# Optimization experiments

Measured on AMD Instinct MI355X. Metric: run time of the kernel, lower is better.

## Reference

```python
import jax, jax.numpy as jnp
import numpy as np
import math

B, S, D = 4, 4096, 2048
HEAD_DIM = 128  # dim_model // head_nums = 2048 // 16
DEPTH = 12


def setup_inputs() -> dict:
    key = jax.random.key(0)
    ks = jax.random.split(key, 8)
    std = 0.1
    return {
        "x": jax.random.normal(ks[0], (B, S, D), dtype=jnp.float32),
        "WQ": jax.random.normal(ks[1], (D, 2 * HEAD_DIM), dtype=jnp.float32) * (D ** -0.5),
        "WK": jax.random.normal(ks[2], (D, 2 * HEAD_DIM), dtype=jnp.float32) * (D ** -0.5),
        "WV": jax.random.normal(ks[3], (D, 2 * HEAD_DIM), dtype=jnp.float32) * (D ** -0.5),
        "lambda_q1": jax.random.normal(ks[4], (HEAD_DIM,), dtype=jnp.float32) * std,
        "lambda_q2": jax.random.normal(ks[5], (HEAD_DIM,), dtype=jnp.float32) * std,
        "lambda_k1": jax.random.normal(ks[6], (HEAD_DIM,), dtype=jnp.float32) * std,
        "lambda_k2": jax.random.normal(ks[7], (HEAD_DIM,), dtype=jnp.float32) * std,
    }


def reference(x, WQ, WK, WV, lambda_q1, lambda_q2, lambda_k1, lambda_k2):
    scale = HEAD_DIM ** -0.5
    lambda_init = 0.8 - 0.6 * math.exp(-0.3 * DEPTH)

    q = x @ WQ                      # [B, S, 2*hd]
    k = x @ WK
    v = x @ WV                      # [B, S, 2*hd]
    q1, q2 = q[..., :HEAD_DIM], q[..., HEAD_DIM:]
    k1, k2 = k[..., :HEAD_DIM], k[..., HEAD_DIM:]

    a1 = jnp.einsum("bqd,bkd->bqk", q1, k1) * scale  # [B, S, S]
    a2 = jnp.einsum("bqd,bkd->bqk", q2, k2) * scale

    lambda_1 = jnp.exp(jnp.sum(lambda_q1 * lambda_k1))
    lambda_2 = jnp.exp(jnp.sum(lambda_q2 * lambda_k2))
    lam = lambda_1 + lambda_2 + lambda_init

    attn = jax.nn.softmax(a1, axis=-1) - lam * jax.nn.softmax(a2, axis=-1)
    return jnp.einsum("bqk,bkd->bqd", attn, v)  # [B, S, 2*hd]
```

## Files before the change

### kernel.cpp

```cpp
#include <hip/hip_runtime.h>
#include <stdint.h>

typedef unsigned short u16;
typedef __attribute__((ext_vector_type(4))) float f32x4;
typedef __attribute__((ext_vector_type(16))) float f32x16;
typedef __attribute__((ext_vector_type(8))) short s16x8;
typedef __attribute__((ext_vector_type(8))) __bf16 bf16x8;
typedef __attribute__((ext_vector_type(8))) unsigned short u16x8;
typedef __attribute__((ext_vector_type(4))) unsigned short u16x4;
typedef __attribute__((ext_vector_type(4))) uint32_t u32x4;

__device__ __forceinline__ f32x4 mfma16(s16x8 a, s16x8 b, f32x4 c) {
  return __builtin_amdgcn_mfma_f32_16x16x32_bf16(
      __builtin_bit_cast(bf16x8, a), __builtin_bit_cast(bf16x8, b), c, 0, 0, 0);
}
__device__ __forceinline__ f32x16 mfma32(s16x8 a, s16x8 b, f32x16 c) {
  return __builtin_amdgcn_mfma_f32_32x32x16_bf16(
      __builtin_bit_cast(bf16x8, a), __builtin_bit_cast(bf16x8, b), c, 0, 0, 0);
}

__device__ __forceinline__ void gl_lds16(const u16* g, u16* l) {
  __builtin_amdgcn_global_load_lds(
      (const __attribute__((address_space(1))) void*)g,
      (__attribute__((address_space(3))) void*)l, 16, 0, 0);
}

__device__ __forceinline__ u16 bf16rne(float f) {
  uint32_t u = __builtin_bit_cast(uint32_t, f);
  u += 0x7fffu + ((u >> 16) & 1u);
  return (u16)(u >> 16);
}

__global__ void cast_x_kernel(const float* __restrict__ x, u16* __restrict__ xb) {
  size_t i = ((size_t)blockIdx.x * 256 + threadIdx.x) * 8;
  f32x4 a = *(const f32x4*)(x + i);
  f32x4 b = *(const f32x4*)(x + i + 4);
  u16x8 o;
#pragma unroll
  for (int j = 0; j < 4; ++j) { o[j] = bf16rne(a[j]); o[4 + j] = bf16rne(b[j]); }
  *(u16x8*)(xb + i) = o;
}

__global__ void cast_w_kernel(const float* __restrict__ WQ, const float* __restrict__ WK,
                              const float* __restrict__ WV, u16* __restrict__ Wt, float qscale) {
  int i = blockIdx.x * 256 + threadIdx.x;
  int r = i >> 11, k = i & 2047;
  int sel = r >> 8, c = r & 255;
  const float* W = (sel == 0) ? WQ : (sel == 1) ? WK : WV;
  float v = W[(size_t)k * 256 + c];
  if (sel == 0) v *= qscale;
  Wt[i] = bf16rne(v);
}

__global__ __launch_bounds__(256) void proj_gemm(const u16* __restrict__ xb, const u16* __restrict__ Wt,
                                                 u16* __restrict__ Qb, u16* __restrict__ Kb,
                                                 u16* __restrict__ Vt) {
  const int bid = blockIdx.x;
  const int xcd = bid & 7, j = bid >> 3;
  const int m0 = (xcd * 16 + (j / 6)) * 128;
  const int n0 = (j % 6) * 128;
  const int tid = threadIdx.x, lane = tid & 63, w = tid >> 6;
  const int ln = lane & 15, quad = lane >> 4;
  const int wm = w & 1, wn = w >> 1;
  __shared__ __align__(16) u16 As[128 * 32];
  __shared__ __align__(16) u16 Bs[128 * 32];
  f32x4 acc[4][4];
#pragma unroll
  for (int i = 0; i < 4; ++i)
#pragma unroll
    for (int jj = 0; jj < 4; ++jj) acc[i][jj] = f32x4{0.f, 0.f, 0.f, 0.f};

  for (int kk = 0; kk < 2048; kk += 32) {
    __syncthreads();
#pragma unroll
    for (int i = 0; i < 2; ++i) {
      int p = tid + i * 256;
      int row = p >> 2, cg = (p & 3) ^ (row & 3);
      gl_lds16(xb + (size_t)(m0 + row) * 2048 + kk + cg * 8, As + (size_t)(p - lane) * 8);
      gl_lds16(Wt + (size_t)(n0 + row) * 2048 + kk + cg * 8, Bs + (size_t)(p - lane) * 8);
    }
    __syncthreads();
    s16x8 a[4];
#pragma unroll
    for (int mt = 0; mt < 4; ++mt) {
      int r = wm * 64 + mt * 16 + ln;
      a[mt] = *(const s16x8*)(As + r * 32 + ((quad ^ (r & 3)) * 8));
    }
#pragma unroll
    for (int nt = 0; nt < 4; ++nt) {
      int r = wn * 64 + nt * 16 + ln;
      s16x8 bf = *(const s16x8*)(Bs + r * 32 + ((quad ^ (r & 3)) * 8));
#pragma unroll
      for (int mt = 0; mt < 4; ++mt) acc[mt][nt] = mfma16(a[mt], bf, acc[mt][nt]);
    }
  }
#pragma unroll
  for (int mt = 0; mt < 4; ++mt)
#pragma unroll
    for (int nt = 0; nt < 4; ++nt) {
      int row0 = m0 + wm * 64 + mt * 16 + quad * 4;
      int col = n0 + wn * 64 + nt * 16 + ln;
      int sel = col >> 8, c = col & 255;
      u16x4 vv;
#pragma unroll
      for (int jj = 0; jj < 4; ++jj) vv[jj] = bf16rne(acc[mt][nt][jj]);
      if (sel == 2) {
        int b = row0 >> 12, s = row0 & 4095;
        *(u16x4*)(Vt + (size_t)b * 1048576 + (size_t)c * 4096 + s) = vv;
      } else {
        u16* dst = (sel == 0) ? Qb : Kb;
#pragma unroll
        for (int jj = 0; jj < 4; ++jj) dst[(size_t)(row0 + jj) * 256 + c] = vv[jj];
      }
    }
}

__global__ void lam_kernel(const float* __restrict__ lq1, const float* __restrict__ lq2,
                           const float* __restrict__ lk1, const float* __restrict__ lk2,
                           float* __restrict__ lamp) {
  int t = threadIdx.x;
  float d1 = lq1[t] * lk1[t] + lq1[t + 64] * lk1[t + 64];
  float d2 = lq2[t] * lk2[t] + lq2[t + 64] * lk2[t + 64];
#pragma unroll
  for (int off = 32; off; off >>= 1) {
    d1 += __shfl_xor(d1, off);
    d2 += __shfl_xor(d2, off);
  }
  if (t == 0) *lamp = expf(d1) + expf(d2) + (0.8f - 0.6f * expf(-3.6f));
}

__global__ __launch_bounds__(256, 2) void attn_kernel(const u16* __restrict__ Qb,
                                                      const u16* __restrict__ Kb,
                                                      const u16* __restrict__ Vt,
                                                      const float* __restrict__ lamp,
                                                      float* __restrict__ out) {
  const int bid = blockIdx.x;
  const int xcd = bid & 7;
  const int b = xcd >> 1;
  const int qt = ((bid >> 3) << 1) + (xcd & 1);
  const int tid = threadIdx.x, lane = tid & 63, w = tid >> 6;
  const int l5 = lane & 31, lh = lane >> 5;
  const int m = w & 1, kt = w >> 1;

  __shared__ __align__(16) char smem[68096];
  u16* Ks = (u16*)smem;
  u16* Vs = (u16*)(smem + 32768);
  float* buf0 = (float*)smem;
  float* buf1 = (float*)(smem + 33792);
  float* ls = (float*)(smem + 67584);

  s16x8 bq[8];
  {
    const u16* qp = Qb + ((size_t)(b * 4096 + qt * 32 + l5)) * 256 + m * 128 + lh * 8;
#pragma unroll
    for (int s = 0; s < 8; ++s) bq[s] = *(const s16x8*)(qp + s * 16);
  }

  f32x16 O[8];
#pragma unroll
  for (int ct = 0; ct < 8; ++ct)
#pragma unroll
    for (int r = 0; r < 16; ++r) O[ct][r] = 0.f;
  float l_run = 0.f;

  const u16* Kg0 = Kb + ((size_t)b * 4096) * 256;
  const u16* Vg0 = Vt + (size_t)b * 1048576;

  for (int kb = 0; kb < 4096; kb += 64) {
    __syncthreads();
#pragma unroll
    for (int i = 0; i < 8; ++i) {
      int p = tid + i * 256;
      int row = p >> 5, c = p & 31;
      int cg = (c & 16) | ((c ^ row) & 15);
      gl_lds16(Kg0 + (size_t)(kb + row) * 256 + cg * 8, Ks + (size_t)(p - lane) * 8);
    }
#pragma unroll
    for (int i = 0; i < 8; ++i) {
      int p = tid + i * 256;
      int row = p >> 3, c = p & 7;
      int cg = c ^ (row & 7);
      gl_lds16(Vg0 + (size_t)row * 4096 + kb + cg * 8, Vs + (size_t)(p - lane) * 8);
    }
    __syncthreads();

    f32x16 Sa, Sb;
#pragma unroll
    for (int r = 0; r < 16; ++r) { Sa[r] = 0.f; Sb[r] = 0.f; }
#pragma unroll
    for (int s = 0; s < 8; s += 2) {
      int row = kt * 32 + l5;
      int c0 = m * 16 + s * 2 + lh;
      int c1 = m * 16 + (s + 1) * 2 + lh;
      s16x8 a0 = *(const s16x8*)(Ks + row * 256 + (((c0 & 16) | ((c0 ^ row) & 15))) * 8);
      s16x8 a1 = *(const s16x8*)(Ks + row * 256 + (((c1 & 16) | ((c1 ^ row) & 15))) * 8);
      Sa = mfma32(a0, bq[s], Sa);
      Sb = mfma32(a1, bq[s + 1], Sb);
    }

    uint32_t P[8];
#pragma unroll
    for (int d = 0; d < 8; ++d) {
      float p0 = exp2f(Sa[2 * d] + Sb[2 * d]);
      float p1 = exp2f(Sa[2 * d + 1] + Sb[2 * d + 1]);
      l_run += p0 + p1;
      P[d] = (uint32_t)bf16rne(p0) | ((uint32_t)bf16rne(p1) << 16);
    }
    uint32_t X[8];
#pragma unroll
    for (int d = 0; d < 8; ++d) X[d] = (uint32_t)__shfl_xor((int)P[d], 32);

#pragma unroll
    for (int ks = 0; ks < 2; ++ks) {
      u32x4 fd;
      fd[0] = lh ? X[ks * 4 + 2] : P[ks * 4 + 0];
      fd[1] = lh ? X[ks * 4 + 3] : P[ks * 4 + 1];
      fd[2] = lh ? P[ks * 4 + 2] : X[ks * 4 + 0];
      fd[3] = lh ? P[ks * 4 + 3] : X[ks * 4 + 1];
      s16x8 pf = __builtin_bit_cast(s16x8, fd);
      int c = (kt * 32 + ks * 16) / 8 + lh;
#pragma unroll
      for (int ct = 0; ct < 8; ++ct) {
        int row = ct * 32 + l5;
        s16x8 vf = *(const s16x8*)(Vs + row * 64 + ((c ^ (row & 7)) * 8));
        O[ct] = mfma32(vf, pf, O[ct]);
      }
    }
  }

  float lam = *lamp;
  l_run += __shfl_xor(l_run, 32);
  __syncthreads();
  if (lane < 32) ls[(m * 2 + kt) * 32 + l5] = l_run;
  float* bufm = m ? buf1 : buf0;
  if (kt == 1) {
#pragma unroll
    for (int ct = 0; ct < 8; ++ct)
#pragma unroll
      for (int r = 0; r < 16; ++r) {
        int vcol = ct * 32 + (r & 3) + 8 * (r >> 2) + 4 * lh;
        bufm[vcol * 33 + l5] = O[ct][r];
      }
  }
  __syncthreads();
  if (kt == 0) {
    float linv = 1.f / (ls[(m * 2) * 32 + l5] + ls[(m * 2 + 1) * 32 + l5]);
#pragma unroll
    for (int ct = 0; ct < 8; ++ct)
#pragma unroll
      for (int r = 0; r < 16; ++r) {
        int vcol = ct * 32 + (r & 3) + 8 * (r >> 2) + 4 * lh;
        bufm[vcol * 33 + l5] = (O[ct][r] + bufm[vcol * 33 + l5]) * linv;
      }
  }
  __syncthreads();
  float* og = out + ((size_t)(b * 4096 + qt * 32)) * 256;
#pragma unroll
  for (int j2 = 0; j2 < 32; ++j2) {
    float v = buf0[tid * 33 + j2] - lam * buf1[tid * 33 + j2];
    og[(size_t)j2 * 256 + tid] = v;
  }
}

extern "C" void kernel_launch(void* const* d_in, const int* in_sizes, int n_in,
                              void* d_out, int out_size, void* d_ws, size_t ws_size,
                              hipStream_t stream) {
  (void)in_sizes; (void)n_in; (void)out_size; (void)ws_size;
  const float* x   = (const float*)d_in[0];
  const float* WQ  = (const float*)d_in[1];
  const float* WK  = (const float*)d_in[2];
  const float* WV  = (const float*)d_in[3];
  const float* lq1 = (const float*)d_in[4];
  const float* lq2 = (const float*)d_in[5];
  const float* lk1 = (const float*)d_in[6];
  const float* lk2 = (const float*)d_in[7];
  float* out = (float*)d_out;

  char* ws = (char*)d_ws;
  u16* xb = (u16*)ws;   ws += (size_t)16384 * 2048 * 2;
  u16* Wt = (u16*)ws;   ws += (size_t)768 * 2048 * 2;
  u16* Qb = (u16*)ws;   ws += (size_t)16384 * 256 * 2;
  u16* Kb = (u16*)ws;   ws += (size_t)16384 * 256 * 2;
  u16* Vt = (u16*)ws;   ws += (size_t)16384 * 256 * 2;
  float* lamp = (float*)ws;

  const float qscale = 0.0883883476f * 1.44269504f;

  hipLaunchKernelGGL(cast_x_kernel, dim3(16384), dim3(256), 0, stream, x, xb);
  hipLaunchKernelGGL(cast_w_kernel, dim3(6144), dim3(256), 0, stream, WQ, WK, WV, Wt, qscale);
  hipLaunchKernelGGL(proj_gemm, dim3(768), dim3(256), 0, stream, xb, Wt, Qb, Kb, Vt);
  hipLaunchKernelGGL(lam_kernel, dim3(1), dim3(64), 0, stream, lq1, lq2, lk1, lk2, lamp);
  hipLaunchKernelGGL(attn_kernel, dim3(512), dim3(256), 0, stream, Qb, Kb, Vt, lamp, out);
}
```

Measured before the change: 442.6 us.

## Double-buffer K/V tiles in LDS, prefetch V fragments, use permlane32_swap

Splits LDS into two 64KB stages so the next K/V tile is fetched with global_load_lds while the current one is computed, leaving one barrier per iteration. V fragments are loaded from LDS into registers before the softmax exp so LDS latency overlaps the exp work. The P transpose across the lane halves uses permlane32_swap instead of shfl_xor plus selects. Launch bounds drop to one block per CU because of the larger LDS footprint and the extra registers, which lowers occupancy.

```diff
diff --git a/kernel.cpp b/kernel.cpp
--- a/kernel.cpp
+++ b/kernel.cpp
@@ -9,6 +9,7 @@
 typedef __attribute__((ext_vector_type(8))) unsigned short u16x8;
 typedef __attribute__((ext_vector_type(4))) unsigned short u16x4;
 typedef __attribute__((ext_vector_type(4))) uint32_t u32x4;
+typedef __attribute__((ext_vector_type(2))) uint32_t u32x2;
 
 __device__ __forceinline__ f32x4 mfma16(s16x8 a, s16x8 b, f32x4 c) {
   return __builtin_amdgcn_mfma_f32_16x16x32_bf16(
@@ -129,7 +130,7 @@
   if (t == 0) *lamp = expf(d1) + expf(d2) + (0.8f - 0.6f * expf(-3.6f));
 }
 
-__global__ __launch_bounds__(256, 2) void attn_kernel(const u16* __restrict__ Qb,
+__global__ __launch_bounds__(256, 1) void attn_kernel(const u16* __restrict__ Qb,
                                                       const u16* __restrict__ Kb,
                                                       const u16* __restrict__ Vt,
                                                       const float* __restrict__ lamp,
@@ -142,32 +143,17 @@
   const int l5 = lane & 31, lh = lane >> 5;
   const int m = w & 1, kt = w >> 1;
 
-  __shared__ __align__(16) char smem[68096];
-  u16* Ks = (u16*)smem;
-  u16* Vs = (u16*)(smem + 32768);
+  __shared__ __align__(16) char smem[131072];
   float* buf0 = (float*)smem;
   float* buf1 = (float*)(smem + 33792);
   float* ls = (float*)(smem + 67584);
 
-  s16x8 bq[8];
-  {
-    const u16* qp = Qb + ((size_t)(b * 4096 + qt * 32 + l5)) * 256 + m * 128 + lh * 8;
-#pragma unroll
-    for (int s = 0; s < 8; ++s) bq[s] = *(const s16x8*)(qp + s * 16);
-  }
-
-  f32x16 O[8];
-#pragma unroll
-  for (int ct = 0; ct < 8; ++ct)
-#pragma unroll
-    for (int r = 0; r < 16; ++r) O[ct][r] = 0.f;
-  float l_run = 0.f;
-
   const u16* Kg0 = Kb + ((size_t)b * 4096) * 256;
   const u16* Vg0 = Vt + (size_t)b * 1048576;
 
-  for (int kb = 0; kb < 4096; kb += 64) {
-    __syncthreads();
+  auto stage = [&](int kb, char* base) {
+    u16* Ks = (u16*)base;
+    u16* Vs = (u16*)(base + 32768);
 #pragma unroll
     for (int i = 0; i < 8; ++i) {
       int p = tid + i * 256;
@@ -182,7 +168,31 @@
       int cg = c ^ (row & 7);
       gl_lds16(Vg0 + (size_t)row * 4096 + kb + cg * 8, Vs + (size_t)(p - lane) * 8);
     }
+  };
+
+  stage(0, smem);
+
+  s16x8 bq[8];
+  {
+    const u16* qp = Qb + ((size_t)(b * 4096 + qt * 32 + l5)) * 256 + m * 128 + lh * 8;
+#pragma unroll
+    for (int s = 0; s < 8; ++s) bq[s] = *(const s16x8*)(qp + s * 16);
+  }
+
+  f32x16 O[8];
+#pragma unroll
+  for (int ct = 0; ct < 8; ++ct)
+#pragma unroll
+    for (int r = 0; r < 16; ++r) O[ct][r] = 0.f;
+  float l_run = 0.f;
+
+  for (int t = 0; t < 64; ++t) {
     __syncthreads();
+    if (t + 1 < 64) stage((t + 1) * 64, smem + ((t + 1) & 1) * 65536);
+
+    char* base = smem + (t & 1) * 65536;
+    u16* Ks = (u16*)base;
+    u16* Vs = (u16*)(base + 32768);
 
     f32x16 Sa, Sb;
 #pragma unroll
@@ -198,6 +208,16 @@
       Sb = mfma32(a1, bq[s + 1], Sb);
     }
 
+    s16x8 vfr0[8], vfr1[8];
+#pragma unroll
+    for (int ct = 0; ct < 8; ++ct) {
+      int row = ct * 32 + l5;
+      int c0v = (kt * 32) / 8 + lh;
+      int c1v = (kt * 32 + 16) / 8 + lh;
+      vfr0[ct] = *(const s16x8*)(Vs + row * 64 + ((c0v ^ (row & 7)) * 8));
+      vfr1[ct] = *(const s16x8*)(Vs + row * 64 + ((c1v ^ (row & 7)) * 8));
+    }
+
     uint32_t P[8];
 #pragma unroll
     for (int d = 0; d < 8; ++d) {
@@ -206,24 +226,20 @@
       l_run += p0 + p1;
       P[d] = (uint32_t)bf16rne(p0) | ((uint32_t)bf16rne(p1) << 16);
     }
-    uint32_t X[8];
-#pragma unroll
-    for (int d = 0; d < 8; ++d) X[d] = (uint32_t)__shfl_xor((int)P[d], 32);
 
 #pragma unroll
     for (int ks = 0; ks < 2; ++ks) {
+      u32x2 s02 = __builtin_amdgcn_permlane32_swap(P[ks * 4 + 0], P[ks * 4 + 2], false, false);
+      u32x2 s13 = __builtin_amdgcn_permlane32_swap(P[ks * 4 + 1], P[ks * 4 + 3], false, false);
       u32x4 fd;
-      fd[0] = lh ? X[ks * 4 + 2] : P[ks * 4 + 0];
-      fd[1] = lh ? X[ks * 4 + 3] : P[ks * 4 + 1];
-      fd[2] = lh ? P[ks * 4 + 2] : X[ks * 4 + 0];
-      fd[3] = lh ? P[ks * 4 + 3] : X[ks * 4 + 1];
+      fd[0] = s02[0]; fd[1] = s13[0]; fd[2] = s02[1]; fd[3] = s13[1];
       s16x8 pf = __builtin_bit_cast(s16x8, fd);
-      int c = (kt * 32 + ks * 16) / 8 + lh;
-#pragma unroll
-      for (int ct = 0; ct < 8; ++ct) {
-        int row = ct * 32 + l5;
-        s16x8 vf = *(const s16x8*)(Vs + row * 64 + ((c ^ (row & 7)) * 8));
-        O[ct] = mfma32(vf, pf, O[ct]);
+      if (ks == 0) {
+#pragma unroll
+        for (int ct = 0; ct < 8; ++ct) O[ct] = mfma32(vfr0[ct], pf, O[ct]);
+      } else {
+#pragma unroll
+        for (int ct = 0; ct < 8; ++ct) O[ct] = mfma32(vfr1[ct], pf, O[ct]);
       }
     }
   }
```

Result: slower. 460.1 us (+4.0%).
